# Kernel optimization log

Measured on AMD Instinct MI355X. Metric: run time of the kernel, lower is better.

Reference implementation:

```python
import jax, jax.numpy as jnp
import numpy as np

N = 20000
CIN = 32
COUT = 64
K = 4              # kernel_size per axis
KF = K * K * K     # 64 kernel bins
EXTENT = 0.1       # filter_extent; search radius = EXTENT/2
E_PAD = 262144
FOUR_OVER_PI = 4.0 / np.pi
EPS = 1e-12


def _safe_sqrt(x):
    # sqrt with zero (not nan) gradient at 0
    return jnp.sqrt(jnp.maximum(x, EPS))


def ball_to_cube_vp(p):
    """Open3D ball_to_cube_volume_preserving: unit ball -> [-1,1]^3 cube.
    p: [E,3] points in the unit ball."""
    x, y, z = p[:, 0], p[:, 1], p[:, 2]
    sq = x * x + y * y + z * z
    norm = _safe_sqrt(sq)
    rxy2 = x * x + y * y
    # --- sphere -> cylinder (volume preserving) ---
    top = 1.25 * z * z > rxy2
    s_top = _safe_sqrt(3.0 * norm / (norm + jnp.abs(z) + EPS))
    s_side = norm / _safe_sqrt(rxy2)
    cx = jnp.where(top, x * s_top, x * s_side)
    cy = jnp.where(top, y * s_top, y * s_side)
    cz = jnp.where(top, jnp.sign(z) * norm, 1.5 * z)
    zero = sq < EPS
    cx = jnp.where(zero, 0.0, cx)
    cy = jnp.where(zero, 0.0, cy)
    cz = jnp.where(zero, 0.0, cz)
    # --- cylinder -> cube (angle preserving square mapping in xy) ---
    rxy = _safe_sqrt(cx * cx + cy * cy)
    xbig = jnp.abs(cy) <= jnp.abs(cx)
    safe_x = jnp.where(jnp.abs(cx) > EPS, cx, 1.0)
    safe_y = jnp.where(jnp.abs(cy) > EPS, cy, 1.0)
    qx = jnp.sign(cx) * rxy
    qy = jnp.sign(cy) * rxy
    bx = jnp.where(xbig, qx, qy * FOUR_OVER_PI * jnp.arctan(cx / safe_y))
    by = jnp.where(xbig, qx * FOUR_OVER_PI * jnp.arctan(cy / safe_x), qy)
    small = cx * cx + cy * cy < EPS
    bx = jnp.where(small, 0.0, bx)
    by = jnp.where(small, 0.0, by)
    return jnp.stack([bx, by, cz], axis=1)


def setup_inputs() -> dict:
    rng = np.random.default_rng(0)
    pos = rng.random((N, 3)).astype(np.float32)
    radius = EXTENT * 0.5
    # chunked brute-force fixed-radius search (ignore self pairs)
    sq_norms = (pos * pos).sum(-1)
    qs, ns = [], []
    chunk = 2000
    for s in range(0, N, chunk):
        blk = pos[s:s + chunk]
        d2 = sq_norms[s:s + chunk, None] + sq_norms[None, :] - 2.0 * blk @ pos.T
        qi, nj = np.nonzero(d2 < radius * radius)
        qi = qi + s
        keep = qi != nj
        qs.append(qi[keep]); ns.append(nj[keep])
    eq = np.concatenate(qs); en = np.concatenate(ns)
    E = eq.shape[0]
    assert E <= E_PAD, E
    edge_q = np.zeros(E_PAD, np.int64); edge_q[:E] = eq
    edge_n = np.zeros(E_PAD, np.int64); edge_n[:E] = en
    edge_valid = np.zeros(E_PAD, np.float32); edge_valid[:E] = 1.0

    key = jax.random.key(0)
    k1, k2, k3, k4 = jax.random.split(key, 4)
    feats = jax.random.normal(k1, (N, CIN), dtype=jnp.float32)
    Wconv = jax.random.normal(k2, (K, K, K, CIN, COUT), dtype=jnp.float32) * 0.05
    Wd = jax.random.normal(k3, (CIN, COUT), dtype=jnp.float32) * 0.05
    bd = jax.random.normal(k4, (COUT,), dtype=jnp.float32) * 0.05
    return {"feats": feats, "pos": jnp.asarray(pos), "Wconv": Wconv,
            "Wd": Wd, "bd": bd,
            "edge_q": jnp.asarray(edge_q), "edge_n": jnp.asarray(edge_n),
            "edge_valid": jnp.asarray(edge_valid)}


def _cconv(feats, pos, Wconv, edge_q, edge_n, edge_valid):
    # relative positions scaled into the unit ball (search radius = EXTENT/2)
    rel = (pos[edge_n] - pos[edge_q]) * (2.0 / EXTENT)          # [E,3]
    cube = ball_to_cube_vp(rel)                                  # [E,3] in [-1,1]^3
    # align_corners=True grid coords
    u = jnp.clip((cube + 1.0) * 0.5 * (K - 1), 0.0, K - 1.0)     # [E,3] (x,y,z)
    i0 = jnp.clip(jnp.floor(u).astype(jnp.int32), 0, K - 2)
    f = u - i0.astype(u.dtype)                                   # trilinear fracs
    fj = feats[edge_n] * edge_valid[:, None]                     # [E,Cin]
    segq = edge_q.astype(jnp.int32) * KF
    # accumulate neighbor feats into per-query kernel bins (8 trilinear corners)
    Z = jnp.zeros((N * KF, CIN), feats.dtype)
    for dz in (0, 1):
        wz = f[:, 2] if dz else 1.0 - f[:, 2]
        for dy in (0, 1):
            wy = f[:, 1] if dy else 1.0 - f[:, 1]
            for dx in (0, 1):
                wx = f[:, 0] if dx else 1.0 - f[:, 0]
                w = wz * wy * wx
                idx = ((i0[:, 2] + dz) * K + (i0[:, 1] + dy)) * K + (i0[:, 0] + dx)
                Z = Z + jax.ops.segment_sum(fj * w[:, None], segq + idx,
                                            num_segments=N * KF)
    # dense contraction against the flattened filter bank
    return jnp.einsum('nki,kio->no', Z.reshape(N, KF, CIN),
                      Wconv.reshape(KF, CIN, COUT))


def reference(feats, pos, Wconv, Wd, bd, edge_q, edge_n, edge_valid):
    ans_conv = _cconv(feats, pos, Wconv, edge_q, edge_n, edge_valid)
    ans_dense = feats @ Wd + bd
    return ans_conv, ans_dense
```

## Files before the change

kernel.cpp:

```cpp
#include <hip/hip_runtime.h>

#define N_PTS 20000
#define CIN   32
#define COUT  64
#define KK    4
#define KF    64
#define KDIM  2048
#define E_PAD 262144
#define EPS   1e-12f
#define FOUR_OVER_PI 1.27323954473516f
#define QB    8
#define MT16  16

#define NB_Q 1024
#define NB_G 1024
#define NB_W 512
#define NB_F 1250
#define NB_D 313

typedef __attribute__((ext_vector_type(8))) short bf16x8;
typedef __attribute__((ext_vector_type(4))) float f32x4;

__device__ __forceinline__ float sgnf(float v) {
    return v > 0.f ? 1.f : (v < 0.f ? -1.f : 0.f);
}
__device__ __forceinline__ int imin(int a, int b) { return a < b ? a : b; }
__device__ __forceinline__ int imax(int a, int b) { return a > b ? a : b; }

__device__ __forceinline__ unsigned short f2bf(float f) {
    unsigned u = __float_as_uint(f);
    u = u + 0x7fffu + ((u >> 16) & 1u);
    return (unsigned short)(u >> 16);
}

__device__ __forceinline__ unsigned cvtpk(float a, float b) {
    unsigned r;
    asm("v_cvt_pk_bf16_f32 %0, %1, %2" : "=v"(r) : "v"(a), "v"(b));
    return r;
}

__device__ __forceinline__ void edge_geom(
    const float* __restrict__ pos, int n, int q,
    int& cellb, float& ofx, float& ofy, float& ofz)
{
    const float rx = (pos[n * 3 + 0] - pos[q * 3 + 0]) * 20.f;
    const float ry = (pos[n * 3 + 1] - pos[q * 3 + 1]) * 20.f;
    const float rz = (pos[n * 3 + 2] - pos[q * 3 + 2]) * 20.f;
    const float sq   = rx * rx + ry * ry + rz * rz;
    const float nrm  = sqrtf(fmaxf(sq, EPS));
    const float rxy2 = rx * rx + ry * ry;
    const bool  top  = (1.25f * rz * rz > rxy2);
    const float s_top  = sqrtf(fmaxf(3.f * nrm / (nrm + fabsf(rz) + EPS), EPS));
    const float s_side = nrm / sqrtf(fmaxf(rxy2, EPS));
    float cx = top ? rx * s_top : rx * s_side;
    float cy = top ? ry * s_top : ry * s_side;
    float cz = top ? sgnf(rz) * nrm : 1.5f * rz;
    if (sq < EPS) { cx = 0.f; cy = 0.f; cz = 0.f; }
    const float rc2 = cx * cx + cy * cy;
    const float rxy = sqrtf(fmaxf(rc2, EPS));
    const bool  xbig = fabsf(cy) <= fabsf(cx);
    const float safe_x = (fabsf(cx) > EPS) ? cx : 1.f;
    const float safe_y = (fabsf(cy) > EPS) ? cy : 1.f;
    const float qxv = sgnf(cx) * rxy;
    const float qyv = sgnf(cy) * rxy;
    float bx = xbig ? qxv : qyv * FOUR_OVER_PI * atanf(cx / safe_y);
    float by = xbig ? qxv * FOUR_OVER_PI * atanf(cy / safe_x) : qyv;
    if (rc2 < EPS) { bx = 0.f; by = 0.f; }
    const float ux = fminf(fmaxf((bx + 1.f) * 0.5f * 3.f, 0.f), 3.f);
    const float uy = fminf(fmaxf((by + 1.f) * 0.5f * 3.f, 0.f), 3.f);
    const float uz = fminf(fmaxf((cz + 1.f) * 0.5f * 3.f, 0.f), 3.f);
    const int ix = imin(imax((int)floorf(ux), 0), 2);
    const int iy = imin(imax((int)floorf(uy), 0), 2);
    const int iz = imin(imax((int)floorf(uz), 0), 2);
    cellb = (iz * KK + iy) * KK + ix;
    ofx = ux - (float)ix; ofy = uy - (float)iy; ofz = uz - (float)iz;
}

__global__ __launch_bounds__(256) void prologue_kernel(
    const float* __restrict__ feats, const float* __restrict__ pos,
    const float* __restrict__ Wconv, const float* __restrict__ Wd,
    const float* __restrict__ bd,
    const int* __restrict__ eq, const int* __restrict__ en,
    const float* __restrict__ ev, int strideQ, int strideN,
    int* __restrict__ qstart, unsigned short* __restrict__ Wfrag,
    unsigned* __restrict__ fbp, float4* __restrict__ rec,
    float* __restrict__ out)
{
    const int bid = blockIdx.x;
    const int tid = threadIdx.x;
    if (bid < NB_Q) {
        const int e = bid * 256 + tid;
        int k = (ev[e] > 0.f) ? eq[e * strideQ] : N_PTS;
        if (k > N_PTS) k = N_PTS;
        int kp = -1;
        if (e > 0) {
            kp = (ev[e - 1] > 0.f) ? eq[(e - 1) * strideQ] : N_PTS;
            if (kp > N_PTS) kp = N_PTS;
        }
        for (int q = kp + 1; q <= k; ++q) qstart[q] = e;
        if (e == E_PAD - 1)
            for (int q = k + 1; q <= N_PTS; ++q) qstart[q] = E_PAD;
    } else if (bid < NB_Q + NB_G) {
        const int e = (bid - NB_Q) * 256 + tid;
        if (ev[e] > 0.f) {
            const int q = eq[e * strideQ];
            const int n = en[e * strideN];
            int ib; float fx, fy, fz;
            edge_geom(pos, n, q, ib, fx, fy, fz);
            float4 r;
            r.x = fx; r.y = fy; r.z = fz;
            r.w = __int_as_float(n | (ib << 16) | (1 << 22));
            rec[e] = r;
        }
    } else if (bid < NB_Q + NB_G + NB_W) {
        const int idx = (bid - NB_Q - NB_G) * 256 + tid;
        const int j    = idx & 7;
        const int lane = (idx >> 3) & 63;
        const int nf   = (idx >> 9) & 3;
        const int ks   = idx >> 11;
        const int k    = ks * 32 + ((lane >> 4) << 3) + j;
        const int col  = nf * 16 + (lane & 15);
        Wfrag[idx] = f2bf(Wconv[k * COUT + col]);
    } else if (bid < NB_Q + NB_G + NB_W + NB_F) {
        const int i = (bid - NB_Q - NB_G - NB_W) * 256 + tid;
        const int n = i >> 4, c = i & 15;
        fbp[i] = cvtpk(feats[n * CIN + c], feats[n * CIN + c + 16]);
    } else {
        const int db   = bid - NB_Q - NB_G - NB_W - NB_F;
        const int wv   = tid >> 6, lane = tid & 63;
        const int r16  = lane & 15, kgrp = lane >> 4;
        const int qb   = (db * 4 + wv) * 16;
        if (qb < N_PTS) {
            const float4 f0 = *(const float4*)(feats + (size_t)(qb + r16) * CIN + kgrp * 8);
            const float4 f1 = *(const float4*)(feats + (size_t)(qb + r16) * CIN + kgrp * 8 + 4);
            bf16x8 a8;
            ((unsigned*)&a8)[0] = cvtpk(f0.x, f0.y);
            ((unsigned*)&a8)[1] = cvtpk(f0.z, f0.w);
            ((unsigned*)&a8)[2] = cvtpk(f1.x, f1.y);
            ((unsigned*)&a8)[3] = cvtpk(f1.z, f1.w);
            #pragma unroll
            for (int nf = 0; nf < 4; ++nf) {
                bf16x8 b8;
                #pragma unroll
                for (int jp = 0; jp < 4; ++jp) {
                    const float w0 = Wd[(kgrp * 8 + jp * 2)     * COUT + nf * 16 + r16];
                    const float w1 = Wd[(kgrp * 8 + jp * 2 + 1) * COUT + nf * 16 + r16];
                    ((unsigned*)&b8)[jp] = cvtpk(w0, w1);
                }
                f32x4 acc = {0.f, 0.f, 0.f, 0.f};
                acc = __builtin_amdgcn_mfma_f32_16x16x32_bf16(a8, b8, acc, 0, 0, 0);
                const float bo = bd[nf * 16 + r16];
                #pragma unroll
                for (int rg = 0; rg < 4; ++rg) {
                    const int q = qb + kgrp * 4 + rg;
                    out[(size_t)N_PTS * COUT + q * COUT + nf * 16 + r16] = acc[rg] + bo;
                }
            }
        }
    }
}

__global__ __launch_bounds__(512, 4) void fused_kernel(
    const unsigned* __restrict__ fbp,
    const float4* __restrict__ rec,
    const unsigned short* __restrict__ Wfrag,
    const int* __restrict__ qstart, float* __restrict__ out)
{
    __shared__ __align__(16) unsigned short Zl[MT16 * KDIM];
    __shared__ __align__(16) char scratch[9216];
    float4 (*ebuf)[2][36]   = (float4 (*)[2][36])scratch;
    float  (*partial)[MT16][COUT] = (float (*)[MT16][COUT])scratch;

    const int t    = threadIdx.x;
    const int w    = t >> 6;
    const int lane = t & 63;
    const int r16  = lane & 15;
    const int kgrp = lane >> 4;
    const int q0   = blockIdx.x * MT16;

    const int dxc = r16 & 3, dyc = r16 >> 2;
    {
        const int qA  = w;
        const int qB  = 15 - w;
        const int lo0 = qstart[q0 + qA];
        const int hi0 = qstart[q0 + qA + 1];
        const int lo1 = qstart[q0 + qB];
        const int hi1 = qstart[q0 + qB + 1];
        const int nch0 = imax(1, (hi0 - lo0 + 31) >> 5);
        const int nch1 = imax(1, (hi1 - lo1 + 31) >> 5);
        const int NC   = nch0 + nch1;

        {
            const int sfi = lane >> 5, l32 = lane & 31;
            const int isq1 = sfi >= nch0;
            const int c    = isq1 ? sfi - nch0 : sfi;
            const int lo   = isq1 ? lo1 : lo0;
            const int hi   = isq1 ? hi1 : hi0;
            const int e    = lo + c * 32 + l32;
            float4 r;
            if (e < hi) r = rec[e];
            else { r.x = 0.f; r.y = 0.f; r.z = 0.f; r.w = __int_as_float(0); }
            ebuf[w][sfi][l32 + (l32 >> 3)] = r;
        }

        f32x4 acc[2][4];
        #pragma unroll
        for (int mf = 0; mf < 2; ++mf)
            #pragma unroll
            for (int nf = 0; nf < 4; ++nf)
                acc[mf][nf] = (f32x4){0.f, 0.f, 0.f, 0.f};

        for (int fi = 0; fi < NC; ++fi) {
            if (fi == nch0) {
                const int qs = qA;
                #pragma unroll
                for (int mf = 0; mf < 2; ++mf)
                    #pragma unroll
                    for (int nf = 0; nf < 4; ++nf) {
                        uint2 dv;
                        dv.x = cvtpk(acc[mf][nf][0], acc[mf][nf][1]);
                        dv.y = cvtpk(acc[mf][nf][2], acc[mf][nf][3]);
                        const int g      = nf * 16 + r16;
                        const int slot   = g * 64 + qs * 4 + mf * 2 + (kgrp >> 1);
                        const int stored = slot ^ (g & 7);
                        *(uint2*)&Zl[stored * 8 + (kgrp & 1) * 4] = dv;
                        acc[mf][nf] = (f32x4){0.f, 0.f, 0.f, 0.f};
                    }
            }
            const float4* buf = ebuf[w][fi & 1];
            bf16x8 bP[4], af[2];
            #pragma unroll
            for (int jp = 0; jp < 4; ++jp) {
                float p[2][4];
                #pragma unroll
                for (int h = 0; h < 2; ++h) {
                    const int j = jp * 2 + h;
                    const float4 r = buf[kgrp * 9 + j];
                    const int meta = __float_as_int(r.w);
                    const int n    = meta & 0xFFFF;
                    const int ib   = (meta >> 16) & 63;
                    const float valid = (meta & (1 << 22)) ? 1.f : 0.f;
                    const int ix = ib & 3, iy = (ib >> 2) & 3, iz = ib >> 4;
                    const float wx = (dxc == ix) ? (1.f - r.x)
                                   : ((dxc == ix + 1) ? r.x : 0.f);
                    const float wy = (dyc == iy) ? (1.f - r.y)
                                   : ((dyc == iy + 1) ? r.y : 0.f);
                    const float wxy = wx * wy * valid;
                    const float z0 = wxy * (1.f - r.z), z1 = wxy * r.z;
                    p[h][0] = (iz == 0) ? z0 : 0.f;
                    p[h][1] = (iz == 0) ? z1 : ((iz == 1) ? z0 : 0.f);
                    p[h][2] = (iz == 2) ? z0 : ((iz == 1) ? z1 : 0.f);
                    p[h][3] = (iz == 2) ? z1 : 0.f;
                    const unsigned uf = fbp[(size_t)n * 16 + r16];
                    af[0][j] = (short)(uf & 0xFFFFu);
                    af[1][j] = (short)(uf >> 16);
                }
                #pragma unroll
                for (int nf = 0; nf < 4; ++nf)
                    ((unsigned*)&bP[nf])[jp] = cvtpk(p[0][nf], p[1][nf]);
            }
            #pragma unroll
            for (int nf = 0; nf < 4; ++nf) {
                acc[0][nf] = __builtin_amdgcn_mfma_f32_16x16x32_bf16(
                    af[0], bP[nf], acc[0][nf], 0, 0, 0);
                acc[1][nf] = __builtin_amdgcn_mfma_f32_16x16x32_bf16(
                    af[1], bP[nf], acc[1][nf], 0, 0, 0);
            }
            const int nfi = fi + 2;
            if (nfi < NC && lane < 32) {
                const int isq1 = nfi >= nch0;
                const int c    = isq1 ? nfi - nch0 : nfi;
                const int lo   = isq1 ? lo1 : lo0;
                const int hi   = isq1 ? hi1 : hi0;
                const int e    = lo + c * 32 + lane;
                float4 r;
                if (e < hi) r = rec[e];
                else { r.x = 0.f; r.y = 0.f; r.z = 0.f;
                       r.w = __int_as_float(0); }
                ebuf[w][fi & 1][lane + (lane >> 3)] = r;
            }
        }
        {
            const int qs = qB;
            #pragma unroll
            for (int mf = 0; mf < 2; ++mf)
                #pragma unroll
                for (int nf = 0; nf < 4; ++nf) {
                    uint2 dv;
                    dv.x = cvtpk(acc[mf][nf][0], acc[mf][nf][1]);
                    dv.y = cvtpk(acc[mf][nf][2], acc[mf][nf][3]);
                    const int g      = nf * 16 + r16;
                    const int slot   = g * 64 + qs * 4 + mf * 2 + (kgrp >> 1);
                    const int stored = slot ^ (g & 7);
                    *(uint2*)&Zl[stored * 8 + (kgrp & 1) * 4] = dv;
                }
        }
    }
    __syncthreads();

    {
        const int kw  = w >> 2;
        const int nfB = w & 3;
        f32x4 acc0 = {0.f, 0.f, 0.f, 0.f};
        f32x4 acc1 = {0.f, 0.f, 0.f, 0.f};
        __builtin_amdgcn_s_setprio(1);
        #pragma unroll 4
        for (int i = 0; i < 16; ++i) {
            const int ksA = kw * 32 + 2 * i;
            const int ksB = ksA + 1;
            const int stA = (ksA * 64 + r16 * 4 + kgrp) ^ (ksA & 7);
            const int stB = (ksB * 64 + r16 * 4 + kgrp) ^ (ksB & 7);
            const bf16x8 aA = *(const bf16x8*)&Zl[stA * 8];
            const bf16x8 aB = *(const bf16x8*)&Zl[stB * 8];
            const bf16x8 bA =
                *(const bf16x8*)(Wfrag + (((ksA * 4 + nfB) * 64) + lane) * 8);
            const bf16x8 bB =
                *(const bf16x8*)(Wfrag + (((ksB * 4 + nfB) * 64) + lane) * 8);
            acc0 = __builtin_amdgcn_mfma_f32_16x16x32_bf16(aA, bA, acc0, 0, 0, 0);
            acc1 = __builtin_amdgcn_mfma_f32_16x16x32_bf16(aB, bB, acc1, 0, 0, 0);
        }
        __builtin_amdgcn_s_setprio(0);
        const f32x4 accB = acc0 + acc1;
        #pragma unroll
        for (int rg = 0; rg < 4; ++rg)
            partial[kw][kgrp * 4 + rg][nfB * 16 + r16] = accB[rg];
    }
    __syncthreads();

    #pragma unroll
    for (int rep = 0; rep < MT16 * COUT / 512; ++rep) {
        const int idx = rep * 512 + t;
        const int r = idx >> 6, o = idx & 63;
        out[(q0 + r) * COUT + o] = partial[0][r][o] + partial[1][r][o];
    }
}

__global__ __launch_bounds__(256) void conv_dense_kernel(
    const float* __restrict__ feats, const float* __restrict__ pos,
    const float* __restrict__ Wconv, const float* __restrict__ Wd,
    const float* __restrict__ bd,
    const int* __restrict__ en, const float* __restrict__ ev,
    const int* __restrict__ qstart, int strideN,
    float* __restrict__ out)
{
    __shared__ float Z[QB][KF][CIN];
    __shared__ float partial[4][QB][COUT];
    __shared__ int   rec_n[256], rec_b[256];
    __shared__ float rec_fx[256], rec_fy[256], rec_fz[256];
    __shared__ int   qs9[QB + 1];

    const int t = threadIdx.x, wave = t >> 6, lane = t & 63;
    const int q0 = blockIdx.x * QB;
    if (t <= QB) qs9[t] = qstart[q0 + t];
    float* zf = &Z[0][0][0];
    for (int j = t; j < QB * KF * CIN; j += 256) zf[j] = 0.f;
    __syncthreads();
    const int eLo = qs9[0], eHi = qs9[QB];
    const int ci = lane & 31, dbase = lane >> 5;
    for (int cb = eLo; cb < eHi; cb += 256) {
        const int cnt = imin(256, eHi - cb);
        if (t < cnt) {
            const int e = cb + t;
            int q = q0;
            #pragma unroll
            for (int s = 1; s < QB; ++s) if (e >= qs9[s]) q = q0 + s;
            int nn = ((const int*)en)[e];
            int ib; float fx, fy, fz;
            edge_geom(pos, nn, q, ib, fx, fy, fz);
            rec_n[t] = nn; rec_b[t] = ib;
            rec_fx[t] = fx; rec_fy[t] = fy; rec_fz[t] = fz;
        }
        __syncthreads();
        for (int s = 0; s < QB / 4; ++s) {
            const int qs = wave * (QB / 4) + s;
            const int lo = imax(qs9[qs], cb);
            const int hi = imin(qs9[qs + 1], cb + cnt);
            for (int e = lo; e < hi; ++e) {
                const int r = e - cb;
                const int n = rec_n[r], ib = rec_b[r];
                const float fx = rec_fx[r], fy = rec_fy[r], fz = rec_fz[r];
                const float fj = feats[n * CIN + ci];
                const float wxf = dbase ? fx : 1.f - fx;
                #pragma unroll
                for (int dd = 0; dd < 4; ++dd) {
                    const int dy = dd & 1, dz = dd >> 1;
                    const float wv = (dz ? fz : 1.f - fz) * (dy ? fy : 1.f - fy) * wxf;
                    Z[qs][ib + dz * 16 + dy * 4 + dbase][ci] += fj * wv;
                }
            }
        }
        __syncthreads();
    }
    float acc[QB];
    #pragma unroll
    for (int qs = 0; qs < QB; ++qs) acc[qs] = 0.f;
    const int o = lane;
    for (int kk = 0; kk < KF / 4; ++kk) {
        const int kf = wave * (KF / 4) + kk;
        #pragma unroll
        for (int ii = 0; ii < CIN; ii += 4) {
            float4 z4[QB];
            #pragma unroll
            for (int qs = 0; qs < QB; ++qs)
                z4[qs] = *(const float4*)&Z[qs][kf][ii];
            #pragma unroll
            for (int c = 0; c < 4; ++c) {
                const float wv = Wconv[(kf * CIN + ii + c) * COUT + o];
                #pragma unroll
                for (int qs = 0; qs < QB; ++qs)
                    acc[qs] += wv * ((const float*)&z4[qs])[c];
            }
        }
    }
    #pragma unroll
    for (int qs = 0; qs < QB; ++qs) partial[wave][qs][o] = acc[qs];
    __syncthreads();
    for (int s = 0; s < QB / 4; ++s) {
        const int qs = wave * (QB / 4) + s;
        const int q  = q0 + qs;
        out[q * COUT + o] = partial[0][qs][o] + partial[1][qs][o] +
                            partial[2][qs][o] + partial[3][qs][o];
        float dacc = bd[o];
        #pragma unroll
        for (int ii = 0; ii < CIN; ++ii)
            dacc += feats[q * CIN + ii] * Wd[ii * COUT + o];
        out[N_PTS * COUT + q * COUT + o] = dacc;
    }
}

__global__ __launch_bounds__(256) void pack_en_kernel(
    const int* __restrict__ en, int stride, int* __restrict__ en32)
{
    const int e = blockIdx.x * 256 + threadIdx.x;
    if (e < E_PAD) en32[e] = en[e * stride];
}

__global__ __launch_bounds__(256) void build_qstart_kernel(
    const int* __restrict__ eq, const float* __restrict__ ev,
    int stride, int* __restrict__ qstart)
{
    int e = blockIdx.x * 256 + threadIdx.x;
    if (e >= E_PAD) return;
    int k = (ev[e] > 0.f) ? eq[e * stride] : N_PTS;
    if (k > N_PTS) k = N_PTS;
    int kp = -1;
    if (e > 0) {
        kp = (ev[e - 1] > 0.f) ? eq[(e - 1) * stride] : N_PTS;
        if (kp > N_PTS) kp = N_PTS;
    }
    for (int q = kp + 1; q <= k; ++q) qstart[q] = e;
    if (e == E_PAD - 1) {
        for (int q = k + 1; q <= N_PTS; ++q) qstart[q] = E_PAD;
    }
}

extern "C" void kernel_launch(void* const* d_in, const int* in_sizes, int n_in,
                              void* d_out, int out_size, void* d_ws, size_t ws_size,
                              hipStream_t stream)
{
    const float* feats = (const float*)d_in[0];
    const float* pos   = (const float*)d_in[1];
    const float* Wconv = (const float*)d_in[2];
    const float* Wd    = (const float*)d_in[3];
    const float* bd    = (const float*)d_in[4];
    const int*   eq    = (const int*)d_in[5];
    const int*   en    = (const int*)d_in[6];
    const float* ev    = (const float*)d_in[7];
    const int strideQ = in_sizes[5] / E_PAD;
    const int strideN = in_sizes[6] / E_PAD;

    int* qstart = (int*)d_ws;
    const size_t offW  = 81920;
    const size_t offFB = offW + 262144;
    const size_t offR  = offFB + (size_t)N_PTS * CIN * 2;
    const size_t needed = offR + (size_t)E_PAD * 16;

    if (ws_size >= needed) {
        unsigned short* Wfrag = (unsigned short*)((char*)d_ws + offW);
        unsigned*       fbp   = (unsigned*)((char*)d_ws + offFB);
        float4*         rec   = (float4*)((char*)d_ws + offR);
        prologue_kernel<<<NB_Q + NB_G + NB_W + NB_F + NB_D, 256, 0, stream>>>(
            feats, pos, Wconv, Wd, bd, eq, en, ev, strideQ, strideN,
            qstart, Wfrag, fbp, rec, (float*)d_out);
        fused_kernel<<<N_PTS / MT16, 512, 0, stream>>>(
            fbp, rec, Wfrag, qstart, (float*)d_out);
    } else {
        build_qstart_kernel<<<E_PAD / 256, 256, 0, stream>>>(
            eq, ev, strideQ, qstart);
        int* en32 = (int*)((char*)d_ws + offW);
        pack_en_kernel<<<E_PAD / 256, 256, 0, stream>>>(en, strideN, en32);
        conv_dense_kernel<<<N_PTS / QB, 256, 0, stream>>>(
            feats, pos, Wconv, Wd, bd, en32, ev, qstart, 1, (float*)d_out);
    }
}
```

Measured before the change: 36.81 us.

## Double fused kernel tile to 32 queries per 1024-thread block

Each block now handles 32 query points with 16 waves instead of 16 with 8 waves. In the second phase every filter fragment loaded from global memory is reused across two 16-row M tiles, which halves Wfrag traffic per query. The K split grows from 2 to 4 partial sums, and the partials are staged in the reused Zl buffer behind an extra barrier. Shared memory roughly doubles to about 137 KB per block, and a 1024-thread block with launch_bounds(1024,4) may limit occupancy and raise register pressure. The grid also shrinks to 625 blocks.

```diff
diff --git a/kernel.cpp b/kernel.cpp
--- a/kernel.cpp
+++ b/kernel.cpp
@@ -10,7 +10,7 @@
 #define EPS   1e-12f
 #define FOUR_OVER_PI 1.27323954473516f
 #define QB    8
-#define MT16  16
+#define MT32  32
 
 #define NB_Q 1024
 #define NB_G 1024
@@ -160,28 +160,26 @@
     }
 }
 
-__global__ __launch_bounds__(512, 4) void fused_kernel(
+__global__ __launch_bounds__(1024, 4) void fused_kernel(
     const unsigned* __restrict__ fbp,
     const float4* __restrict__ rec,
     const unsigned short* __restrict__ Wfrag,
     const int* __restrict__ qstart, float* __restrict__ out)
 {
-    __shared__ __align__(16) unsigned short Zl[MT16 * KDIM];
-    __shared__ __align__(16) char scratch[9216];
-    float4 (*ebuf)[2][36]   = (float4 (*)[2][36])scratch;
-    float  (*partial)[MT16][COUT] = (float (*)[MT16][COUT])scratch;
+    __shared__ __align__(16) unsigned short Zl[MT32 * KDIM];
+    __shared__ __align__(16) float4 ebuf[16][2][36];
 
     const int t    = threadIdx.x;
     const int w    = t >> 6;
     const int lane = t & 63;
     const int r16  = lane & 15;
     const int kgrp = lane >> 4;
-    const int q0   = blockIdx.x * MT16;
+    const int q0   = blockIdx.x * MT32;
 
     const int dxc = r16 & 3, dyc = r16 >> 2;
     {
         const int qA  = w;
-        const int qB  = 15 - w;
+        const int qB  = 31 - w;
         const int lo0 = qstart[q0 + qA];
         const int hi0 = qstart[q0 + qA + 1];
         const int lo1 = qstart[q0 + qB];
@@ -221,13 +219,13 @@
                         dv.x = cvtpk(acc[mf][nf][0], acc[mf][nf][1]);
                         dv.y = cvtpk(acc[mf][nf][2], acc[mf][nf][3]);
                         const int g      = nf * 16 + r16;
-                        const int slot   = g * 64 + qs * 4 + mf * 2 + (kgrp >> 1);
+                        const int slot   = g * 128 + qs * 4 + mf * 2 + (kgrp >> 1);
                         const int stored = slot ^ (g & 7);
                         *(uint2*)&Zl[stored * 8 + (kgrp & 1) * 4] = dv;
                         acc[mf][nf] = (f32x4){0.f, 0.f, 0.f, 0.f};
                     }
             }
-            const float4* buf = ebuf[w][fi & 1];
+            const float4* buf = &ebuf[w][fi & 1][0];
             bf16x8 bP[4], af[2];
             #pragma unroll
             for (int jp = 0; jp < 4; ++jp) {
@@ -290,7 +288,7 @@
                     dv.x = cvtpk(acc[mf][nf][0], acc[mf][nf][1]);
                     dv.y = cvtpk(acc[mf][nf][2], acc[mf][nf][3]);
                     const int g      = nf * 16 + r16;
-                    const int slot   = g * 64 + qs * 4 + mf * 2 + (kgrp >> 1);
+                    const int slot   = g * 128 + qs * 4 + mf * 2 + (kgrp >> 1);
                     const int stored = slot ^ (g & 7);
                     *(uint2*)&Zl[stored * 8 + (kgrp & 1) * 4] = dv;
                 }
@@ -298,40 +296,47 @@
     }
     __syncthreads();
 
+    f32x4 accB[2];
     {
-        const int kw  = w >> 2;
+        const int kq  = w >> 2;
         const int nfB = w & 3;
-        f32x4 acc0 = {0.f, 0.f, 0.f, 0.f};
-        f32x4 acc1 = {0.f, 0.f, 0.f, 0.f};
+        accB[0] = (f32x4){0.f, 0.f, 0.f, 0.f};
+        accB[1] = (f32x4){0.f, 0.f, 0.f, 0.f};
         __builtin_amdgcn_s_setprio(1);
         #pragma unroll 4
         for (int i = 0; i < 16; ++i) {
-            const int ksA = kw * 32 + 2 * i;
-            const int ksB = ksA + 1;
-            const int stA = (ksA * 64 + r16 * 4 + kgrp) ^ (ksA & 7);
-            const int stB = (ksB * 64 + r16 * 4 + kgrp) ^ (ksB & 7);
-            const bf16x8 aA = *(const bf16x8*)&Zl[stA * 8];
-            const bf16x8 aB = *(const bf16x8*)&Zl[stB * 8];
-            const bf16x8 bA =
-                *(const bf16x8*)(Wfrag + (((ksA * 4 + nfB) * 64) + lane) * 8);
-            const bf16x8 bB =
-                *(const bf16x8*)(Wfrag + (((ksB * 4 + nfB) * 64) + lane) * 8);
-            acc0 = __builtin_amdgcn_mfma_f32_16x16x32_bf16(aA, bA, acc0, 0, 0, 0);
-            acc1 = __builtin_amdgcn_mfma_f32_16x16x32_bf16(aB, bB, acc1, 0, 0, 0);
+            const int ks = kq * 16 + i;
+            const bf16x8 b =
+                *(const bf16x8*)(Wfrag + (((ks * 4 + nfB) * 64) + lane) * 8);
+            const int st0 = (ks * 128 + r16 * 4 + kgrp) ^ (ks & 7);
+            const int st1 = (ks * 128 + (16 + r16) * 4 + kgrp) ^ (ks & 7);
+            const bf16x8 a0 = *(const bf16x8*)&Zl[st0 * 8];
+            const bf16x8 a1 = *(const bf16x8*)&Zl[st1 * 8];
+            accB[0] = __builtin_amdgcn_mfma_f32_16x16x32_bf16(a0, b, accB[0], 0, 0, 0);
+            accB[1] = __builtin_amdgcn_mfma_f32_16x16x32_bf16(a1, b, accB[1], 0, 0, 0);
         }
         __builtin_amdgcn_s_setprio(0);
-        const f32x4 accB = acc0 + acc1;
+    }
+    __syncthreads();
+
+    {
+        float (*partial)[MT32][COUT] = (float (*)[MT32][COUT])Zl;
+        const int kq  = w >> 2;
+        const int nfB = w & 3;
         #pragma unroll
-        for (int rg = 0; rg < 4; ++rg)
-            partial[kw][kgrp * 4 + rg][nfB * 16 + r16] = accB[rg];
-    }
-    __syncthreads();
-
-    #pragma unroll
-    for (int rep = 0; rep < MT16 * COUT / 512; ++rep) {
-        const int idx = rep * 512 + t;
-        const int r = idx >> 6, o = idx & 63;
-        out[(q0 + r) * COUT + o] = partial[0][r][o] + partial[1][r][o];
+        for (int mh = 0; mh < 2; ++mh)
+            #pragma unroll
+            for (int rg = 0; rg < 4; ++rg)
+                partial[kq][mh * 16 + kgrp * 4 + rg][nfB * 16 + r16] =
+                    accB[mh][rg];
+        __syncthreads();
+        #pragma unroll
+        for (int rep = 0; rep < MT32 * COUT / 1024; ++rep) {
+            const int idx = rep * 1024 + t;
+            const int r = idx >> 6, o = idx & 63;
+            out[(q0 + r) * COUT + o] = partial[0][r][o] + partial[1][r][o] +
+                                       partial[2][r][o] + partial[3][r][o];
+        }
     }
 }
 
@@ -482,7 +487,7 @@
         prologue_kernel<<<NB_Q + NB_G + NB_W + NB_F + NB_D, 256, 0, stream>>>(
             feats, pos, Wconv, Wd, bd, eq, en, ev, strideQ, strideN,
             qstart, Wfrag, fbp, rec, (float*)d_out);
-        fused_kernel<<<N_PTS / MT16, 512, 0, stream>>>(
+        fused_kernel<<<N_PTS / MT32, 1024, 0, stream>>>(
             fbp, rec, Wfrag, qstart, (float*)d_out);
     } else {
         build_qstart_kernel<<<E_PAD / 256, 256, 0, stream>>>(
```

Result: slower. 40.49 us (+10.0%).

## Process adjacent query pair as one merged edge stream with dual accumulators

Applied to the files above, without the earlier changes.

Each wave now handles queries 2w and 2w+1 as one contiguous edge range rather than queries w and 15-w as two separately padded chunk streams. A flag bit marks which query each edge belongs to, and the trilinear weights are split into two masked B operands feeding separate accumulator sets. This cuts the padding waste from rounding each query up to 32 edges, but it doubles the MFMA count per chunk and the accumulator registers, and it drops the w/15-w pairing that balanced load across waves.

```diff
diff --git a/kernel.cpp b/kernel.cpp
--- a/kernel.cpp
+++ b/kernel.cpp
@@ -180,58 +180,38 @@
 
     const int dxc = r16 & 3, dyc = r16 >> 2;
     {
-        const int qA  = w;
-        const int qB  = 15 - w;
-        const int lo0 = qstart[q0 + qA];
-        const int hi0 = qstart[q0 + qA + 1];
-        const int lo1 = qstart[q0 + qB];
-        const int hi1 = qstart[q0 + qB + 1];
-        const int nch0 = imax(1, (hi0 - lo0 + 31) >> 5);
-        const int nch1 = imax(1, (hi1 - lo1 + 31) >> 5);
-        const int NC   = nch0 + nch1;
+        const int lo  = qstart[q0 + 2 * w];
+        const int mid = qstart[q0 + 2 * w + 1];
+        const int hi  = qstart[q0 + 2 * w + 2];
+        const int NC  = imax(1, (hi - lo + 31) >> 5);
 
         {
             const int sfi = lane >> 5, l32 = lane & 31;
-            const int isq1 = sfi >= nch0;
-            const int c    = isq1 ? sfi - nch0 : sfi;
-            const int lo   = isq1 ? lo1 : lo0;
-            const int hi   = isq1 ? hi1 : hi0;
-            const int e    = lo + c * 32 + l32;
+            const int e   = lo + sfi * 32 + l32;
             float4 r;
             if (e < hi) r = rec[e];
             else { r.x = 0.f; r.y = 0.f; r.z = 0.f; r.w = __int_as_float(0); }
+            int meta = __float_as_int(r.w);
+            if (e < mid) meta |= (1 << 23);
+            r.w = __int_as_float(meta);
             ebuf[w][sfi][l32 + (l32 >> 3)] = r;
         }
 
-        f32x4 acc[2][4];
+        f32x4 accA[2][4], accB[2][4];
         #pragma unroll
         for (int mf = 0; mf < 2; ++mf)
             #pragma unroll
-            for (int nf = 0; nf < 4; ++nf)
-                acc[mf][nf] = (f32x4){0.f, 0.f, 0.f, 0.f};
+            for (int nf = 0; nf < 4; ++nf) {
+                accA[mf][nf] = (f32x4){0.f, 0.f, 0.f, 0.f};
+                accB[mf][nf] = (f32x4){0.f, 0.f, 0.f, 0.f};
+            }
 
         for (int fi = 0; fi < NC; ++fi) {
-            if (fi == nch0) {
-                const int qs = qA;
-                #pragma unroll
-                for (int mf = 0; mf < 2; ++mf)
-                    #pragma unroll
-                    for (int nf = 0; nf < 4; ++nf) {
-                        uint2 dv;
-                        dv.x = cvtpk(acc[mf][nf][0], acc[mf][nf][1]);
-                        dv.y = cvtpk(acc[mf][nf][2], acc[mf][nf][3]);
-                        const int g      = nf * 16 + r16;
-                        const int slot   = g * 64 + qs * 4 + mf * 2 + (kgrp >> 1);
-                        const int stored = slot ^ (g & 7);
-                        *(uint2*)&Zl[stored * 8 + (kgrp & 1) * 4] = dv;
-                        acc[mf][nf] = (f32x4){0.f, 0.f, 0.f, 0.f};
-                    }
-            }
-            const float4* buf = ebuf[w][fi & 1];
-            bf16x8 bP[4], af[2];
+            const float4* buf = &ebuf[w][fi & 1][0];
+            bf16x8 bPA[4], bPB[4], af[2];
             #pragma unroll
             for (int jp = 0; jp < 4; ++jp) {
-                float p[2][4];
+                float pA[2][4], pB[2][4];
                 #pragma unroll
                 for (int h = 0; h < 2; ++h) {
                     const int j = jp * 2 + h;
@@ -240,6 +220,7 @@
                     const int n    = meta & 0xFFFF;
                     const int ib   = (meta >> 16) & 63;
                     const float valid = (meta & (1 << 22)) ? 1.f : 0.f;
+                    const float selA  = (meta & (1 << 23)) ? 1.f : 0.f;
                     const int ix = ib & 3, iy = (ib >> 2) & 3, iz = ib >> 4;
                     const float wx = (dxc == ix) ? (1.f - r.x)
                                    : ((dxc == ix + 1) ? r.x : 0.f);
@@ -247,48 +228,59 @@
                                    : ((dyc == iy + 1) ? r.y : 0.f);
                     const float wxy = wx * wy * valid;
                     const float z0 = wxy * (1.f - r.z), z1 = wxy * r.z;
-                    p[h][0] = (iz == 0) ? z0 : 0.f;
-                    p[h][1] = (iz == 0) ? z1 : ((iz == 1) ? z0 : 0.f);
-                    p[h][2] = (iz == 2) ? z0 : ((iz == 1) ? z1 : 0.f);
-                    p[h][3] = (iz == 2) ? z1 : 0.f;
+                    float p0 = (iz == 0) ? z0 : 0.f;
+                    float p1 = (iz == 0) ? z1 : ((iz == 1) ? z0 : 0.f);
+                    float p2 = (iz == 2) ? z0 : ((iz == 1) ? z1 : 0.f);
+                    float p3 = (iz == 2) ? z1 : 0.f;
+                    pA[h][0] = p0 * selA;  pB[h][0] = p0 - pA[h][0];
+                    pA[h][1] = p1 * selA;  pB[h][1] = p1 - pA[h][1];
+                    pA[h][2] = p2 * selA;  pB[h][2] = p2 - pA[h][2];
+                    pA[h][3] = p3 * selA;  pB[h][3] = p3 - pA[h][3];
                     const unsigned uf = fbp[(size_t)n * 16 + r16];
                     af[0][j] = (short)(uf & 0xFFFFu);
                     af[1][j] = (short)(uf >> 16);
                 }
                 #pragma unroll
-                for (int nf = 0; nf < 4; ++nf)
-                    ((unsigned*)&bP[nf])[jp] = cvtpk(p[0][nf], p[1][nf]);
+                for (int nf = 0; nf < 4; ++nf) {
+                    ((unsigned*)&bPA[nf])[jp] = cvtpk(pA[0][nf], pA[1][nf]);
+                    ((unsigned*)&bPB[nf])[jp] = cvtpk(pB[0][nf], pB[1][nf]);
+                }
             }
             #pragma unroll
             for (int nf = 0; nf < 4; ++nf) {
-                acc[0][nf] = __builtin_amdgcn_mfma_f32_16x16x32_bf16(
-                    af[0], bP[nf], acc[0][nf], 0, 0, 0);
-                acc[1][nf] = __builtin_amdgcn_mfma_f32_16x16x32_bf16(
-                    af[1], bP[nf], acc[1][nf], 0, 0, 0);
+                accA[0][nf] = __builtin_amdgcn_mfma_f32_16x16x32_bf16(
+                    af[0], bPA[nf], accA[0][nf], 0, 0, 0);
+                accA[1][nf] = __builtin_amdgcn_mfma_f32_16x16x32_bf16(
+                    af[1], bPA[nf], accA[1][nf], 0, 0, 0);
+                accB[0][nf] = __builtin_amdgcn_mfma_f32_16x16x32_bf16(
+                    af[0], bPB[nf], accB[0][nf], 0, 0, 0);
+                accB[1][nf] = __builtin_amdgcn_mfma_f32_16x16x32_bf16(
+                    af[1], bPB[nf], accB[1][nf], 0, 0, 0);
             }
             const int nfi = fi + 2;
             if (nfi < NC && lane < 32) {
-                const int isq1 = nfi >= nch0;
-                const int c    = isq1 ? nfi - nch0 : nfi;
-                const int lo   = isq1 ? lo1 : lo0;
-                const int hi   = isq1 ? hi1 : hi0;
-                const int e    = lo + c * 32 + lane;
+                const int e = lo + nfi * 32 + lane;
                 float4 r;
                 if (e < hi) r = rec[e];
                 else { r.x = 0.f; r.y = 0.f; r.z = 0.f;
                        r.w = __int_as_float(0); }
+                int meta = __float_as_int(r.w);
+                if (e < mid) meta |= (1 << 23);
+                r.w = __int_as_float(meta);
                 ebuf[w][fi & 1][lane + (lane >> 3)] = r;
             }
         }
-        {
-            const int qs = qB;
+        #pragma unroll
+        for (int half = 0; half < 2; ++half) {
+            const int qs = 2 * w + half;
             #pragma unroll
             for (int mf = 0; mf < 2; ++mf)
                 #pragma unroll
                 for (int nf = 0; nf < 4; ++nf) {
+                    const f32x4 a = half ? accB[mf][nf] : accA[mf][nf];
                     uint2 dv;
-                    dv.x = cvtpk(acc[mf][nf][0], acc[mf][nf][1]);
-                    dv.y = cvtpk(acc[mf][nf][2], acc[mf][nf][3]);
+                    dv.x = cvtpk(a[0], a[1]);
+                    dv.y = cvtpk(a[2], a[3]);
                     const int g      = nf * 16 + r16;
                     const int slot   = g * 64 + qs * 4 + mf * 2 + (kgrp >> 1);
                     const int stored = slot ^ (g & 7);
```

Result: faster. 34.66 us (-5.8%).
